# Kernel tuning notes

Hardware: AMD Instinct MI355X
Metric: run time of the kernel (lower is better)

Reference implementation:

```python
import jax, jax.numpy as jnp
import numpy as np

BN_EPS = 1e-5
B, L, D = 16, 2048, 1024
OS = 64          # attnList[0]
NC = 256         # candidates per sample
CLASS_NUM = 8921
LAB = 1024


def setup_inputs() -> dict:
    key = jax.random.key(0)
    ks = jax.random.split(key, 8)
    scale_a = 1.0 / np.sqrt(D)
    return {
        "X": jax.random.normal(ks[0], (B, L, D), jnp.float32),
        "candidate": jax.random.randint(ks[1], (B, NC), 0, CLASS_NUM, jnp.int64),
        "a_w": jax.random.normal(ks[2], (D, OS), jnp.float32) * scale_a,
        "a_b": jnp.zeros((OS,), jnp.float32),
        "h_w": jax.random.normal(ks[3], (D, LAB), jnp.float32) * scale_a,
        "h_b": jnp.zeros((LAB,), jnp.float32),
        "bn_gamma": jax.random.uniform(ks[4], (LAB,), jnp.float32, 0.5, 1.5),
        "bn_beta": jax.random.normal(ks[5], (LAB,), jnp.float32) * 0.1,
        "bn_mean": jnp.zeros((LAB,), jnp.float32),
        "bn_var": jnp.ones((LAB,), jnp.float32),
        "labDescVec": jax.random.normal(ks[6], (CLASS_NUM, LAB), jnp.float32),
    }


def reference(X, candidate, a_w, a_b, h_w, h_b, bn_gamma, bn_beta, bn_mean, bn_var, labDescVec):
    # --- attention-pooling layer (attnList has one entry) ---
    # alpha: softmax over the sequence dim (dim=1 in torch)
    alpha = jax.nn.softmax(jnp.einsum('bld,do->blo', X, a_w) + a_b, axis=1)  # [B,L,OS]
    Xp = jnp.einsum('blo,bld->bod', alpha, X)                                # [B,OS,D]
    Xp = jnp.einsum('bod,dh->boh', Xp, h_w) + h_b                            # [B,OS,LAB]
    # BatchNorm1d over feature dim (eval mode: running stats)
    Xp = (Xp - bn_mean) * (bn_gamma / jnp.sqrt(bn_var + BN_EPS)) + bn_beta
    Xp = jax.nn.relu(Xp)  # dropout is identity at inference
    # --- candidate attention ---
    batchLabelVec = labDescVec[candidate]                                    # [B,NC,LAB]
    scores = jnp.einsum('boh,bch->boc', Xp, batchLabelVec)                   # [B,OS,NC]
    alpha2 = jax.nn.softmax(scores, axis=1)                                  # softmax over OS (dim=1)
    out = jnp.einsum('boc,boh->bch', alpha2, Xp)                             # [B,NC,LAB]
    return out
```

## Files before the change

### kernel.cpp

```cpp
#include <hip/hip_runtime.h>
#include <hip/hip_bf16.h>
#include <math.h>

#define Bb   16
#define Ll   2048
#define Dd   1024
#define OSo  64
#define NCc  256
#define LABh 1024
#define BN_EPS 1e-5f

typedef short s8v  __attribute__((ext_vector_type(8)));
typedef short s4v  __attribute__((ext_vector_type(4)));
typedef float f32x4 __attribute__((ext_vector_type(4)));

__device__ __forceinline__ short f2b(float f) {
    __hip_bfloat16 h = __float2bfloat16(f);
    short s;
    __builtin_memcpy(&s, &h, 2);
    return s;
}
__device__ __forceinline__ float b2f(short s) {
    union { unsigned u; float f; } v; v.u = ((unsigned)(unsigned short)s) << 16;
    return v.f;
}
__device__ __forceinline__ void g2lds16(const void* g, void* l) {
    __builtin_amdgcn_global_load_lds(
        (const __attribute__((address_space(1))) void*)g,
        (__attribute__((address_space(3))) void*)l, 16, 0, 0);
}
__device__ __forceinline__ void fastbar() {
    asm volatile("s_waitcnt lgkmcnt(0)\n\ts_barrier" ::: "memory");
}
__device__ __forceinline__ void dmabar6() {
    asm volatile("s_waitcnt vmcnt(6) lgkmcnt(0)\n\ts_barrier" ::: "memory");
}
__device__ __forceinline__ void dmabar0() {
    asm volatile("s_waitcnt vmcnt(0) lgkmcnt(0)\n\ts_barrier" ::: "memory");
}
__device__ __forceinline__ int swi(int row, int kElem) {
    return (row * 128 + ((kElem * 2) ^ ((row & 7) << 4))) >> 1;
}
__device__ __forceinline__ f32x4 MF(s8v a, s8v b, f32x4 c) {
    return __builtin_amdgcn_mfma_f32_16x16x32_bf16(a, b, c, 0, 0, 0);
}

__global__ __launch_bounds__(256) void k0(const float* __restrict__ h_w,
                                          const float* __restrict__ a_w,
                                          short* __restrict__ h_wT,
                                          short* __restrict__ a_wT) {
    __shared__ float t[64][68];
    const int tid = threadIdx.x, id = blockIdx.x;
    const float* src; short* dst; int srw, d0, y0;
    if (id < 256) { src = h_w; dst = h_wT; srw = LABh; d0 = (id & 15) * 64; y0 = (id >> 4) * 64; }
    else          { src = a_w; dst = a_wT; srw = OSo;  d0 = (id - 256) * 64; y0 = 0; }
    const int r = tid >> 2, cofs = (tid & 3) * 16;
    #pragma unroll
    for (int w = 0; w < 4; ++w) {
        float4 v = *(const float4*)&src[(size_t)(d0 + r) * srw + y0 + cofs + w * 4];
        t[r][cofs + w * 4 + 0] = v.x;
        t[r][cofs + w * 4 + 1] = v.y;
        t[r][cofs + w * 4 + 2] = v.z;
        t[r][cofs + w * 4 + 3] = v.w;
    }
    __syncthreads();
    s8v o0, o1;
    #pragma unroll
    for (int e = 0; e < 8; ++e) { o0[e] = f2b(t[cofs + e][r]); o1[e] = f2b(t[cofs + 8 + e][r]); }
    *(s8v*)&dst[(size_t)(y0 + r) * Dd + d0 + cofs]     = o0;
    *(s8v*)&dst[(size_t)(y0 + r) * Dd + d0 + cofs + 8] = o1;
}

__global__ __launch_bounds__(256) void k1(const float* __restrict__ X,
                                          const short* __restrict__ a_wT,
                                          float* __restrict__ St) {
    __shared__ __align__(16) char smem[49152];
    float (*ts)[65] = (float(*)[65])smem;
    const int tid = threadIdx.x, lane = tid & 63, wave = tid >> 6;
    const int wm = wave >> 1, wn = wave & 1;
    const int b = blockIdx.y, l0 = blockIdx.x * 64;
    const float* Xb = X + ((size_t)b * Ll + l0) * Dd;
    const int akb = (lane & 15) * 16;
    const int bkb = (lane & 7) * 16;
    f32x4 acc[2][2] = {};

    auto issue = [&](int t, int k0) {
        char* Ab = smem + (t & 1) * 16384;
        #pragma unroll
        for (int q = 0; q < 4; ++q) {
            const int chunk = wave * 4 + q;
            const int row = chunk * 4 + (lane >> 4);
            const char* g = (const char*)Xb + (size_t)row * 4096 + k0 * 4
                          + (akb ^ ((row & 7) << 4));
            g2lds16(g, Ab + chunk * 1024);
        }
        char* Bbuf = smem + 32768 + (t & 1) * 8192;
        #pragma unroll
        for (int q = 0; q < 2; ++q) {
            const int chunk = wave * 2 + q;
            const int row = chunk * 8 + (lane >> 3);
            const char* g = (const char*)a_wT + (size_t)row * 2048 + k0 * 2
                          + (bkb ^ ((row & 7) << 4));
            g2lds16(g, Bbuf + chunk * 1024);
        }
    };

    issue(0, 0);
    #pragma unroll
    for (int t = 0; t < 16; ++t) {
        if (t < 15) { issue(t + 1, (t + 1) * 64); dmabar6(); }
        else        { dmabar0(); }
        const char* Ab = smem + (t & 1) * 16384;
        const char* Bbuf = smem + 32768 + (t & 1) * 8192;
        #pragma unroll
        for (int kk = 0; kk < 2; ++kk) {
            s8v a[2], bv[2];
            #pragma unroll
            for (int i = 0; i < 2; ++i) {
                const int row = wm * 32 + i * 16 + (lane & 15);
                const int sw = (row & 7) << 4;
                const int kbyte = kk * 128 + (lane >> 4) * 32;
                float4 v0 = *(const float4*)(Ab + row * 256 + ((kbyte) ^ sw));
                float4 v1 = *(const float4*)(Ab + row * 256 + ((kbyte + 16) ^ sw));
                s8v s;
                s[0]=f2b(v0.x); s[1]=f2b(v0.y); s[2]=f2b(v0.z); s[3]=f2b(v0.w);
                s[4]=f2b(v1.x); s[5]=f2b(v1.y); s[6]=f2b(v1.z); s[7]=f2b(v1.w);
                a[i] = s;
            }
            #pragma unroll
            for (int j = 0; j < 2; ++j) {
                const int row = wn * 32 + j * 16 + (lane & 15);
                const int sw = (row & 7) << 4;
                const int kbyte = kk * 64 + (lane >> 4) * 16;
                bv[j] = *(const s8v*)(Bbuf + row * 128 + (kbyte ^ sw));
            }
            #pragma unroll
            for (int i = 0; i < 2; ++i)
                #pragma unroll
                for (int j = 0; j < 2; ++j)
                    acc[i][j] = MF(a[i], bv[j], acc[i][j]);
        }
        fastbar();
    }
    __syncthreads();
    #pragma unroll
    for (int i = 0; i < 2; ++i)
        #pragma unroll
        for (int j = 0; j < 2; ++j)
            #pragma unroll
            for (int rr = 0; rr < 4; ++rr)
                ts[wm * 32 + i * 16 + (lane >> 4) * 4 + rr][wn * 32 + j * 16 + (lane & 15)] = acc[i][j][rr];
    __syncthreads();
    const int o = tid >> 2, lofs = (tid & 3) * 16;
    float* Sp = St + ((size_t)b * OSo + o) * Ll + l0 + lofs;
    #pragma unroll
    for (int w = 0; w < 4; ++w) {
        float4 v;
        v.x = ts[lofs + w * 4 + 0][o];
        v.y = ts[lofs + w * 4 + 1][o];
        v.z = ts[lofs + w * 4 + 2][o];
        v.w = ts[lofs + w * 4 + 3][o];
        *(float4*)&Sp[w * 4] = v;
    }
}

__global__ __launch_bounds__(256) void k2(const float* __restrict__ St,
                                          const float* __restrict__ a_b,
                                          short* __restrict__ aBf) {
    __shared__ float row[Ll];
    __shared__ float red[8];
    const float* p0 = St + (size_t)blockIdx.x * Ll;
    short* ab = aBf + (size_t)blockIdx.x * Ll;
    const int tid = threadIdx.x;
    const int wave = tid >> 6, lane = tid & 63;
    const float bias = a_b[blockIdx.x & (OSo - 1)];
    const int base = tid * 4;
    float m = -1e30f;
    #pragma unroll
    for (int i = base; i < Ll; i += 1024) {
        float4 a = *(const float4*)&p0[i];
        float4 v;
        v.x = a.x + bias; v.y = a.y + bias;
        v.z = a.z + bias; v.w = a.w + bias;
        *(float4*)&row[i] = v;
        m = fmaxf(m, fmaxf(fmaxf(v.x, v.y), fmaxf(v.z, v.w)));
    }
    #pragma unroll
    for (int off = 32; off; off >>= 1) m = fmaxf(m, __shfl_down(m, off));
    if (lane == 0) red[wave] = m;
    __syncthreads();
    if (tid == 0) red[4] = fmaxf(fmaxf(red[0], red[1]), fmaxf(red[2], red[3]));
    __syncthreads();
    const float M = red[4];
    float s = 0.f;
    #pragma unroll
    for (int i = base; i < Ll; i += 1024) {
        float4 v = *(const float4*)&row[i];
        v.x = __expf(v.x - M); v.y = __expf(v.y - M);
        v.z = __expf(v.z - M); v.w = __expf(v.w - M);
        *(float4*)&row[i] = v;
        s += (v.x + v.y) + (v.z + v.w);
    }
    __syncthreads();
    #pragma unroll
    for (int off = 32; off; off >>= 1) s += __shfl_down(s, off);
    if (lane == 0) red[wave] = s;
    __syncthreads();
    if (tid == 0) red[4] = 1.f / (red[0] + red[1] + red[2] + red[3]);
    __syncthreads();
    const float inv = red[4];
    #pragma unroll
    for (int i = base; i < Ll; i += 1024) {
        float4 v = *(const float4*)&row[i];
        s4v o;
        o[0] = f2b(v.x * inv); o[1] = f2b(v.y * inv);
        o[2] = f2b(v.z * inv); o[3] = f2b(v.w * inv);
        *(s4v*)&ab[i] = o;
    }
}

struct R3 { s8v al[2]; float4 xv[4]; };

__global__ __launch_bounds__(256) void k3(const float* __restrict__ X,
                                          const short* __restrict__ aBf,
                                          short* __restrict__ XpP) {
    __shared__ __align__(16) char smem[32768];
    float (*ts)[68] = (float(*)[68])smem;
    const int tid = threadIdx.x;
    const int lane = tid & 63, wave = tid >> 6;
    const int wm = wave >> 1, wn = wave & 1;
    const int id = blockIdx.x;
    const int slot = id >> 3;
    const int b = (id & 7) * 2 + (slot >> 5);
    const int inner = slot & 31;
    const int dt = inner & 15, z = inner >> 4;
    const int d0 = dt * 64;
    const float* Xb = X + (size_t)b * Ll * Dd;
    const short* ab = aBf + (size_t)b * OSo * Ll;
    short* outP = XpP + (size_t)z * ((size_t)Bb * OSo * Dd);
    f32x4 acc[2][2] = {};
    const int arow = tid >> 2, akofs = (tid & 3) * 16;
    const int lq = tid & 15, dq = tid >> 4;
    const int lbase = z * 1024;
    R3 cur, nxt;
    #pragma unroll
    for (int w = 0; w < 2; ++w)
        cur.al[w] = *(const s8v*)&ab[(size_t)arow * Ll + lbase + akofs + w * 8];
    #pragma unroll
    for (int i = 0; i < 4; ++i)
        cur.xv[i] = *(const float4*)&Xb[(size_t)(lbase + lq * 4 + i) * Dd + d0 + dq * 4];
    #pragma unroll
    for (int t = 0; t < 16; ++t) {
        short* Aal = (short*)(smem + (t & 1) * 8192);
        short* Xs  = (short*)(smem + 16384 + (t & 1) * 8192);
        #pragma unroll
        for (int w = 0; w < 2; ++w)
            *(s8v*)&Aal[swi(arow, akofs + w * 8)] = cur.al[w];
        {
            const float* f = (const float*)cur.xv;
            #pragma unroll
            for (int j = 0; j < 4; ++j) {
                const int rowd = dq * 4 + j;
                s4v sj;
                sj[0] = f2b(f[0 * 4 + j]);
                sj[1] = f2b(f[1 * 4 + j]);
                sj[2] = f2b(f[2 * 4 + j]);
                sj[3] = f2b(f[3 * 4 + j]);
                *(s4v*)&Xs[swi(rowd, lq * 4)] = sj;
            }
        }
        fastbar();
        if (t < 15) {
            const int l0 = lbase + (t + 1) * 64;
            #pragma unroll
            for (int w = 0; w < 2; ++w)
                nxt.al[w] = *(const s8v*)&ab[(size_t)arow * Ll + l0 + akofs + w * 8];
            #pragma unroll
            for (int i = 0; i < 4; ++i)
                nxt.xv[i] = *(const float4*)&Xb[(size_t)(l0 + lq * 4 + i) * Dd + d0 + dq * 4];
        }
        #pragma unroll
        for (int kk = 0; kk < 2; ++kk) {
            const int kb = kk * 32 + (lane >> 4) * 8;
            s8v a[2], bb[2];
            #pragma unroll
            for (int i = 0; i < 2; ++i)
                a[i] = *(const s8v*)&Aal[swi(wm * 32 + i * 16 + (lane & 15), kb)];
            #pragma unroll
            for (int j = 0; j < 2; ++j)
                bb[j] = *(const s8v*)&Xs[swi(wn * 32 + j * 16 + (lane & 15), kb)];
            #pragma unroll
            for (int i = 0; i < 2; ++i)
                #pragma unroll
                for (int j = 0; j < 2; ++j)
                    acc[i][j] = MF(a[i], bb[j], acc[i][j]);
        }
        if (t < 15) cur = nxt;
    }
    __syncthreads();
    #pragma unroll
    for (int i = 0; i < 2; ++i)
        #pragma unroll
        for (int j = 0; j < 2; ++j)
            #pragma unroll
            for (int rr = 0; rr < 4; ++rr)
                ts[wm * 32 + i * 16 + (lane >> 4) * 4 + rr][wn * 32 + j * 16 + (lane & 15)] = acc[i][j][rr];
    __syncthreads();
    const int o = tid >> 2, dofs = (tid & 3) * 16;
    short* op = outP + ((size_t)b * OSo + o) * Dd + d0 + dofs;
    #pragma unroll
    for (int w = 0; w < 2; ++w) {
        float4 v0 = *(const float4*)&ts[o][dofs + w * 8];
        float4 v1 = *(const float4*)&ts[o][dofs + w * 8 + 4];
        s8v s;
        s[0]=f2b(v0.x); s[1]=f2b(v0.y); s[2]=f2b(v0.z); s[3]=f2b(v0.w);
        s[4]=f2b(v1.x); s[5]=f2b(v1.y); s[6]=f2b(v1.z); s[7]=f2b(v1.w);
        *(s8v*)&op[w * 8] = s;
    }
}

struct R4 { s8v p[4]; s8v w[2]; };

__global__ __launch_bounds__(256) void k4(const short* __restrict__ XpP,
                                          const short* __restrict__ h_wT,
                                          const float* __restrict__ h_b,
                                          const float* __restrict__ gamma,
                                          const float* __restrict__ beta,
                                          const float* __restrict__ mean,
                                          const float* __restrict__ var,
                                          short* __restrict__ Xh) {
    __shared__ __align__(16) char smem[32768];
    short* tsb = (short*)smem;
    const int tid = threadIdx.x, lane = tid & 63, wave = tid >> 6;
    const int wm = wave >> 1, wn = wave & 1;
    const int id = blockIdx.x;
    const int slot = id >> 3;
    const int mt = (id & 7) * 2 + (slot >> 4);
    const int ht = slot & 15;
    const int h0 = ht * 64, m0 = mt * 64;
    const int r = tid >> 2, kofs = (tid & 3) * 16;
    const size_t ZS = (size_t)Bb * OSo * Dd;
    f32x4 acc[2][2] = {};
    R4 cur, nxt;
    #pragma unroll
    for (int w = 0; w < 2; ++w) {
        const short* p0 = XpP + (size_t)(m0 + r) * Dd + kofs + w * 8;
        cur.p[w*2]   = *(const s8v*)&p0[0];
        cur.p[w*2+1] = *(const s8v*)&p0[ZS];
        cur.w[w]     = *(const s8v*)&h_wT[(size_t)(h0 + r) * Dd + kofs + w * 8];
    }
    #pragma unroll
    for (int t = 0; t < 16; ++t) {
        short* As = (short*)(smem + (t & 1) * 8192);
        short* Bs = (short*)(smem + 16384 + (t & 1) * 8192);
        #pragma unroll
        for (int w = 0; w < 2; ++w) {
            s8v q0 = cur.p[w*2], q1 = cur.p[w*2+1];
            s8v s;
            #pragma unroll
            for (int e = 0; e < 8; ++e) s[e] = f2b(b2f(q0[e]) + b2f(q1[e]));
            *(s8v*)&As[swi(r, kofs + w * 8)] = s;
            *(s8v*)&Bs[swi(r, kofs + w * 8)] = cur.w[w];
        }
        fastbar();
        if (t < 15) {
            const int k0 = (t + 1) * 64;
            #pragma unroll
            for (int w = 0; w < 2; ++w) {
                const short* p0 = XpP + (size_t)(m0 + r) * Dd + k0 + kofs + w * 8;
                nxt.p[w*2]   = *(const s8v*)&p0[0];
                nxt.p[w*2+1] = *(const s8v*)&p0[ZS];
                nxt.w[w]     = *(const s8v*)&h_wT[(size_t)(h0 + r) * Dd + k0 + kofs + w * 8];
            }
        }
        #pragma unroll
        for (int kk = 0; kk < 2; ++kk) {
            const int kb = kk * 32 + (lane >> 4) * 8;
            s8v a[2], bb[2];
            #pragma unroll
            for (int i = 0; i < 2; ++i)
                a[i] = *(const s8v*)&As[swi(wm * 32 + i * 16 + (lane & 15), kb)];
            #pragma unroll
            for (int j = 0; j < 2; ++j)
                bb[j] = *(const s8v*)&Bs[swi(wn * 32 + j * 16 + (lane & 15), kb)];
            #pragma unroll
            for (int i = 0; i < 2; ++i)
                #pragma unroll
                for (int j = 0; j < 2; ++j)
                    acc[i][j] = MF(a[i], bb[j], acc[i][j]);
        }
        if (t < 15) cur = nxt;
    }
    __syncthreads();
    #pragma unroll
    for (int j = 0; j < 2; ++j) {
        const int h = h0 + wn * 32 + j * 16 + (lane & 15);
        const float sc = gamma[h] * rsqrtf(var[h] + BN_EPS);
        const float of = (h_b[h] - mean[h]) * sc + beta[h];
        #pragma unroll
        for (int i = 0; i < 2; ++i)
            #pragma unroll
            for (int rr = 0; rr < 4; ++rr) {
                const int ml = wm * 32 + i * 16 + (lane >> 4) * 4 + rr;
                tsb[ml * 64 + wn * 32 + j * 16 + (lane & 15)] = f2b(fmaxf(0.f, acc[i][j][rr] * sc + of));
            }
    }
    __syncthreads();
    #pragma unroll
    for (int w = 0; w < 2; ++w)
        *(s8v*)&Xh[(size_t)(m0 + r) * LABh + h0 + kofs + w * 8] = *(const s8v*)&tsb[r * 64 + kofs + w * 8];
}

struct R56 { float4 ld; s8v xh[2]; };

__global__ __launch_bounds__(256) void k56(const int* __restrict__ cand,
                                           const float* __restrict__ labD,
                                           const short* __restrict__ Xh,
                                           float* __restrict__ out) {
    __shared__ __align__(16) char smem[20608];
    float (*ts)[68] = (float(*)[68])smem;
    float (*al)[64] = (float(*)[64])(smem + 4608);
    int* cidx = (int*)(smem + 20480);
    const int tid = threadIdx.x, lane = tid & 63, wave = tid >> 6;
    const int id = blockIdx.x;
    const int slot = id >> 3;
    const int b = (id & 7) * 2 + (slot >> 4);
    const int c0 = (slot & 15) * 16;
    if (tid < 16) cidx[tid] = cand[b * NCc + c0 + tid];
    __syncthreads();
    const int ar = tid >> 4, ak = (tid & 15) * 4;
    const int br = tid >> 2, bk = (tid & 3) * 16;
    const float* lrow = labD + (size_t)cidx[ar] * LABh;
    const short* xb = Xh + (size_t)b * OSo * LABh;
    f32x4 acc = {};
    R56 cur, nxt;
    cur.ld    = *(const float4*)&lrow[ak];
    cur.xh[0] = *(const s8v*)&xb[(size_t)br * LABh + bk];
    cur.xh[1] = *(const s8v*)&xb[(size_t)br * LABh + bk + 8];
    #pragma unroll
    for (int t = 0; t < 16; ++t) {
        short* As = (short*)(smem + (t & 1) * 10240);
        short* Bs = As + 1024;
        {
            s4v sa;
            sa[0] = f2b(cur.ld.x); sa[1] = f2b(cur.ld.y);
            sa[2] = f2b(cur.ld.z); sa[3] = f2b(cur.ld.w);
            *(s4v*)&As[swi(ar, ak)] = sa;
            *(s8v*)&Bs[swi(br, bk)]     = cur.xh[0];
            *(s8v*)&Bs[swi(br, bk + 8)] = cur.xh[1];
        }
        fastbar();
        if (t < 15) {
            const int k0 = (t + 1) * 64;
            nxt.ld    = *(const float4*)&lrow[k0 + ak];
            nxt.xh[0] = *(const s8v*)&xb[(size_t)br * LABh + k0 + bk];
            nxt.xh[1] = *(const s8v*)&xb[(size_t)br * LABh + k0 + bk + 8];
        }
        #pragma unroll
        for (int kk = 0; kk < 2; ++kk) {
            const int kb = kk * 32 + (lane >> 4) * 8;
            s8v a  = *(const s8v*)&As[swi(lane & 15, kb)];
            s8v bv = *(const s8v*)&Bs[swi(wave * 16 + (lane & 15), kb)];
            acc = MF(a, bv, acc);
        }
        if (t < 15) cur = nxt;
    }
    __syncthreads();
    #pragma unroll
    for (int rr = 0; rr < 4; ++rr)
        ts[(lane >> 4) * 4 + rr][wave * 16 + (lane & 15)] = acc[rr];
    __syncthreads();
    {
        const int cl = tid >> 4, t16 = tid & 15;
        float v[4];
        float m = -1e30f;
        #pragma unroll
        for (int j = 0; j < 4; ++j) { v[j] = ts[cl][t16 + j * 16]; m = fmaxf(m, v[j]); }
        #pragma unroll
        for (int off = 8; off; off >>= 1) m = fmaxf(m, __shfl_xor(m, off, 16));
        float s = 0.f;
        #pragma unroll
        for (int j = 0; j < 4; ++j) { v[j] = __expf(v[j] - m); s += v[j]; }
        #pragma unroll
        for (int off = 8; off; off >>= 1) s += __shfl_xor(s, off, 16);
        const float inv = 1.f / s;
        #pragma unroll
        for (int j = 0; j < 4; ++j) al[cl][t16 + j * 16] = v[j] * inv;
    }
    __syncthreads();
    const int h0 = tid * 4;
    float acc2[16][4] = {};
    for (int o = 0; o < OSo; ++o) {
        s4v xv = *(const s4v*)&xb[(size_t)o * LABh + h0];
        const float x0 = b2f(xv[0]), x1 = b2f(xv[1]), x2 = b2f(xv[2]), x3 = b2f(xv[3]);
        #pragma unroll
        for (int c = 0; c < 16; ++c) {
            const float w = al[c][o];
            acc2[c][0] += w * x0; acc2[c][1] += w * x1;
            acc2[c][2] += w * x2; acc2[c][3] += w * x3;
        }
    }
    #pragma unroll
    for (int c = 0; c < 16; ++c) {
        float4 v; v.x = acc2[c][0]; v.y = acc2[c][1]; v.z = acc2[c][2]; v.w = acc2[c][3];
        *(float4*)&out[((size_t)b * NCc + c0 + c) * LABh + h0] = v;
    }
}

extern "C" void kernel_launch(void* const* d_in, const int* in_sizes, int n_in,
                              void* d_out, int out_size, void* d_ws, size_t ws_size,
                              hipStream_t stream) {
    (void)in_sizes; (void)n_in; (void)out_size; (void)ws_size;
    const float* X      = (const float*)d_in[0];
    const int*   cand   = (const int*)  d_in[1];
    const float* a_w    = (const float*)d_in[2];
    const float* a_b    = (const float*)d_in[3];
    const float* h_w    = (const float*)d_in[4];
    const float* h_b    = (const float*)d_in[5];
    const float* gamma  = (const float*)d_in[6];
    const float* beta   = (const float*)d_in[7];
    const float* mean   = (const float*)d_in[8];
    const float* var    = (const float*)d_in[9];
    const float* labDesc= (const float*)d_in[10];
    float* outp = (float*)d_out;

    char* ws = (char*)d_ws;
    float* St   = (float*)ws;
    short* XpP  = (short*)ws;
    short* aBf  = (short*)(ws + ((size_t)16 << 20));
    short* Xh   = (short*)(ws + ((size_t)20 << 20));
    short* a_wT = (short*)(ws + ((size_t)26 << 20));
    short* h_wT = (short*)(ws + ((size_t)27 << 20));

    k0 <<<272,          256, 0, stream>>>(h_w, a_w, h_wT, a_wT);
    k1 <<<dim3(32, 16), 256, 0, stream>>>(X, a_wT, St);
    k2 <<<Bb * OSo,     256, 0, stream>>>(St, a_b, aBf);
    k3 <<<512,          256, 0, stream>>>(X, aBf, XpP);
    k4 <<<256,          256, 0, stream>>>(XpP, h_wT, h_b, gamma, beta, mean, var, Xh);
    k56<<<256,          256, 0, stream>>>(cand, labDesc, Xh, outp);
}
```

Measured before the change: 94.48 us.

## Stream k4 and k56 operand tiles via direct global-to-LDS DMA

The k4 and k56 main loops now load their operand tiles with global_load_lds (buffer-to-LDS DMA) into double-buffered, XOR-swizzled shared memory, instead of staging them through registers and then writing to LDS. In k4 the two partial Xp halves are now summed after the LDS read rather than before the write. In k56 the fp32 label rows are converted to bf16 after the LDS read. The aim is to cut register pressure and VALU/LDS-write work and to overlap the next tile's loads with the current MFMAs. In exchange, k4 uses more LDS (48KB), which may lower occupancy, and the conversion and add work is now repeated per wave on the read side.

```diff
diff --git a/kernel.cpp b/kernel.cpp
--- a/kernel.cpp
+++ b/kernel.cpp
@@ -34,6 +34,9 @@
 }
 __device__ __forceinline__ void dmabar6() {
     asm volatile("s_waitcnt vmcnt(6) lgkmcnt(0)\n\ts_barrier" ::: "memory");
+}
+__device__ __forceinline__ void dmabar3() {
+    asm volatile("s_waitcnt vmcnt(3) lgkmcnt(0)\n\ts_barrier" ::: "memory");
 }
 __device__ __forceinline__ void dmabar0() {
     asm volatile("s_waitcnt vmcnt(0) lgkmcnt(0)\n\ts_barrier" ::: "memory");
@@ -319,8 +322,6 @@
     }
 }
 
-struct R4 { s8v p[4]; s8v w[2]; };
-
 __global__ __launch_bounds__(256) void k4(const short* __restrict__ XpP,
                                           const short* __restrict__ h_wT,
                                           const float* __restrict__ h_b,
@@ -329,7 +330,7 @@
                                           const float* __restrict__ mean,
                                           const float* __restrict__ var,
                                           short* __restrict__ Xh) {
-    __shared__ __align__(16) char smem[32768];
+    __shared__ __align__(16) char smem[49152];
     short* tsb = (short*)smem;
     const int tid = threadIdx.x, lane = tid & 63, wave = tid >> 6;
     const int wm = wave >> 1, wn = wave & 1;
@@ -338,58 +339,60 @@
     const int mt = (id & 7) * 2 + (slot >> 4);
     const int ht = slot & 15;
     const int h0 = ht * 64, m0 = mt * 64;
-    const int r = tid >> 2, kofs = (tid & 3) * 16;
     const size_t ZS = (size_t)Bb * OSo * Dd;
+    const short* P0g = XpP + (size_t)m0 * Dd;
+    const short* P1g = P0g + ZS;
+    const short* Bg  = h_wT + (size_t)h0 * Dd;
     f32x4 acc[2][2] = {};
-    R4 cur, nxt;
-    #pragma unroll
-    for (int w = 0; w < 2; ++w) {
-        const short* p0 = XpP + (size_t)(m0 + r) * Dd + kofs + w * 8;
-        cur.p[w*2]   = *(const s8v*)&p0[0];
-        cur.p[w*2+1] = *(const s8v*)&p0[ZS];
-        cur.w[w]     = *(const s8v*)&h_wT[(size_t)(h0 + r) * Dd + kofs + w * 8];
-    }
+
+    auto issue = [&](int t, int k0) {
+        char* base = smem + (t & 1) * 24576;
+        #pragma unroll
+        for (int q = 0; q < 2; ++q) {
+            const int chunk = wave * 2 + q;
+            const int row = chunk * 8 + (lane >> 3);
+            const int byt = ((lane & 7) * 16) ^ ((row & 7) << 4);
+            g2lds16((const char*)P0g + (size_t)row * 2048 + k0 * 2 + byt, base + chunk * 1024);
+            g2lds16((const char*)P1g + (size_t)row * 2048 + k0 * 2 + byt, base + 8192 + chunk * 1024);
+            g2lds16((const char*)Bg  + (size_t)row * 2048 + k0 * 2 + byt, base + 16384 + chunk * 1024);
+        }
+    };
+
+    issue(0, 0);
     #pragma unroll
     for (int t = 0; t < 16; ++t) {
-        short* As = (short*)(smem + (t & 1) * 8192);
-        short* Bs = (short*)(smem + 16384 + (t & 1) * 8192);
-        #pragma unroll
-        for (int w = 0; w < 2; ++w) {
-            s8v q0 = cur.p[w*2], q1 = cur.p[w*2+1];
-            s8v s;
-            #pragma unroll
-            for (int e = 0; e < 8; ++e) s[e] = f2b(b2f(q0[e]) + b2f(q1[e]));
-            *(s8v*)&As[swi(r, kofs + w * 8)] = s;
-            *(s8v*)&Bs[swi(r, kofs + w * 8)] = cur.w[w];
-        }
-        fastbar();
-        if (t < 15) {
-            const int k0 = (t + 1) * 64;
-            #pragma unroll
-            for (int w = 0; w < 2; ++w) {
-                const short* p0 = XpP + (size_t)(m0 + r) * Dd + k0 + kofs + w * 8;
-                nxt.p[w*2]   = *(const s8v*)&p0[0];
-                nxt.p[w*2+1] = *(const s8v*)&p0[ZS];
-                nxt.w[w]     = *(const s8v*)&h_wT[(size_t)(h0 + r) * Dd + k0 + kofs + w * 8];
+        if (t < 15) { issue(t + 1, (t + 1) * 64); dmabar6(); }
+        else        { dmabar0(); }
+        const char* base = smem + (t & 1) * 24576;
+        #pragma unroll
+        for (int kk = 0; kk < 2; ++kk) {
+            s8v a[2], bv[2];
+            #pragma unroll
+            for (int i = 0; i < 2; ++i) {
+                const int row = wm * 32 + i * 16 + (lane & 15);
+                const int sw = (row & 7) << 4;
+                const int kbyte = kk * 64 + (lane >> 4) * 16;
+                s8v q0 = *(const s8v*)(base + row * 128 + (kbyte ^ sw));
+                s8v q1 = *(const s8v*)(base + 8192 + row * 128 + (kbyte ^ sw));
+                s8v s;
+                #pragma unroll
+                for (int e = 0; e < 8; ++e) s[e] = f2b(b2f(q0[e]) + b2f(q1[e]));
+                a[i] = s;
             }
-        }
-        #pragma unroll
-        for (int kk = 0; kk < 2; ++kk) {
-            const int kb = kk * 32 + (lane >> 4) * 8;
-            s8v a[2], bb[2];
-            #pragma unroll
-            for (int i = 0; i < 2; ++i)
-                a[i] = *(const s8v*)&As[swi(wm * 32 + i * 16 + (lane & 15), kb)];
-            #pragma unroll
-            for (int j = 0; j < 2; ++j)
-                bb[j] = *(const s8v*)&Bs[swi(wn * 32 + j * 16 + (lane & 15), kb)];
+            #pragma unroll
+            for (int j = 0; j < 2; ++j) {
+                const int row = wn * 32 + j * 16 + (lane & 15);
+                const int sw = (row & 7) << 4;
+                const int kbyte = kk * 64 + (lane >> 4) * 16;
+                bv[j] = *(const s8v*)(base + 16384 + row * 128 + (kbyte ^ sw));
+            }
             #pragma unroll
             for (int i = 0; i < 2; ++i)
                 #pragma unroll
                 for (int j = 0; j < 2; ++j)
-                    acc[i][j] = MF(a[i], bb[j], acc[i][j]);
-        }
-        if (t < 15) cur = nxt;
+                    acc[i][j] = MF(a[i], bv[j], acc[i][j]);
+        }
+        fastbar();
     }
     __syncthreads();
     #pragma unroll
@@ -406,21 +409,20 @@
             }
     }
     __syncthreads();
+    const int r = tid >> 2, kofs = (tid & 3) * 16;
     #pragma unroll
     for (int w = 0; w < 2; ++w)
         *(s8v*)&Xh[(size_t)(m0 + r) * LABh + h0 + kofs + w * 8] = *(const s8v*)&tsb[r * 64 + kofs + w * 8];
 }
-
-struct R56 { float4 ld; s8v xh[2]; };
 
 __global__ __launch_bounds__(256) void k56(const int* __restrict__ cand,
                                            const float* __restrict__ labD,
                                            const short* __restrict__ Xh,
                                            float* __restrict__ out) {
-    __shared__ __align__(16) char smem[20608];
+    __shared__ __align__(16) char smem[28800];
     float (*ts)[68] = (float(*)[68])smem;
-    float (*al)[64] = (float(*)[64])(smem + 4608);
-    int* cidx = (int*)(smem + 20480);
+    float (*al)[64] = (float(*)[64])(smem + 24576);
+    int* cidx = (int*)(smem + 28672);
     const int tid = threadIdx.x, lane = tid & 63, wave = tid >> 6;
     const int id = blockIdx.x;
     const int slot = id >> 3;
@@ -428,42 +430,45 @@
     const int c0 = (slot & 15) * 16;
     if (tid < 16) cidx[tid] = cand[b * NCc + c0 + tid];
     __syncthreads();
-    const int ar = tid >> 4, ak = (tid & 15) * 4;
-    const int br = tid >> 2, bk = (tid & 3) * 16;
-    const float* lrow = labD + (size_t)cidx[ar] * LABh;
     const short* xb = Xh + (size_t)b * OSo * LABh;
+    const int arow = wave * 4 + (lane >> 4);
+    const char* aSrc = (const char*)(labD + (size_t)cidx[arow] * LABh)
+                     + (((lane & 15) * 16) ^ ((arow & 7) << 4));
     f32x4 acc = {};
-    R56 cur, nxt;
-    cur.ld    = *(const float4*)&lrow[ak];
-    cur.xh[0] = *(const s8v*)&xb[(size_t)br * LABh + bk];
-    cur.xh[1] = *(const s8v*)&xb[(size_t)br * LABh + bk + 8];
+
+    auto issue = [&](int t, int k0) {
+        char* base = smem + (t & 1) * 12288;
+        g2lds16(aSrc + k0 * 4, base + wave * 1024);
+        #pragma unroll
+        for (int q = 0; q < 2; ++q) {
+            const int chunk = wave * 2 + q;
+            const int row = chunk * 8 + (lane >> 3);
+            const int byt = ((lane & 7) * 16) ^ ((row & 7) << 4);
+            g2lds16((const char*)xb + (size_t)row * 2048 + k0 * 2 + byt, base + 4096 + chunk * 1024);
+        }
+    };
+
+    issue(0, 0);
     #pragma unroll
     for (int t = 0; t < 16; ++t) {
-        short* As = (short*)(smem + (t & 1) * 10240);
-        short* Bs = As + 1024;
-        {
-            s4v sa;
-            sa[0] = f2b(cur.ld.x); sa[1] = f2b(cur.ld.y);
-            sa[2] = f2b(cur.ld.z); sa[3] = f2b(cur.ld.w);
-            *(s4v*)&As[swi(ar, ak)] = sa;
-            *(s8v*)&Bs[swi(br, bk)]     = cur.xh[0];
-            *(s8v*)&Bs[swi(br, bk + 8)] = cur.xh[1];
+        if (t < 15) { issue(t + 1, (t + 1) * 64); dmabar3(); }
+        else        { dmabar0(); }
+        const char* base = smem + (t & 1) * 12288;
+        #pragma unroll
+        for (int kk = 0; kk < 2; ++kk) {
+            const int ar = lane & 15, swa = (ar & 7) << 4;
+            const int kbyteA = kk * 128 + (lane >> 4) * 32;
+            float4 v0 = *(const float4*)(base + ar * 256 + (kbyteA ^ swa));
+            float4 v1 = *(const float4*)(base + ar * 256 + ((kbyteA + 16) ^ swa));
+            s8v a;
+            a[0]=f2b(v0.x); a[1]=f2b(v0.y); a[2]=f2b(v0.z); a[3]=f2b(v0.w);
+            a[4]=f2b(v1.x); a[5]=f2b(v1.y); a[6]=f2b(v1.z); a[7]=f2b(v1.w);
+            const int br = wave * 16 + (lane & 15), swb = (br & 7) << 4;
+            const int kbyteB = kk * 64 + (lane >> 4) * 16;
+            s8v bv = *(const s8v*)(base + 4096 + br * 128 + (kbyteB ^ swb));
+            acc = MF(a, bv, acc);
         }
         fastbar();
-        if (t < 15) {
-            const int k0 = (t + 1) * 64;
-            nxt.ld    = *(const float4*)&lrow[k0 + ak];
-            nxt.xh[0] = *(const s8v*)&xb[(size_t)br * LABh + k0 + bk];
-            nxt.xh[1] = *(const s8v*)&xb[(size_t)br * LABh + k0 + bk + 8];
-        }
-        #pragma unroll
-        for (int kk = 0; kk < 2; ++kk) {
-            const int kb = kk * 32 + (lane >> 4) * 8;
-            s8v a  = *(const s8v*)&As[swi(lane & 15, kb)];
-            s8v bv = *(const s8v*)&Bs[swi(wave * 16 + (lane & 15), kb)];
-            acc = MF(a, bv, acc);
-        }
-        if (t < 15) cur = nxt;
     }
     __syncthreads();
     #pragma unroll
```

New measurement: 96.04 us. No clear change (+1.7%).
